# Optimization experiments

Hardware: AMD Instinct MI355X
Metric: run time of the kernel (lower is better)

Reference implementation:

```python
import jax, jax.numpy as jnp
import numpy as np

B, H, W, C = 16, 64, 64, 256
DIRECTIONS = [(0, -1), (1, -1), (1, 0), (1, 1), (0, 1), (-1, 1), (-1, 0), (-1, -1)]


def _shift(g, dx, dy):
    # zero-padded shift matching the torch _shift_grid semantics:
    # result[:, max(0,dy):H+min(0,dy), max(0,dx):W+min(0,dx)] = g[src slices]
    _, h, w, _ = g.shape
    padded = jnp.pad(g, ((0, 0), (max(0, dy), max(0, -dy)), (max(0, dx), max(0, -dx)), (0, 0)))
    return padded[:, max(0, -dy):max(0, -dy) + h, max(0, -dx):max(0, -dx) + w, :]


def setup_inputs() -> dict:
    key = jax.random.key(0)
    k1, k2, k3, k4 = jax.random.split(key, 4)
    grid_embedding = jax.random.normal(k1, (B, H, W, C), dtype=jnp.float32)
    Wd = jax.random.normal(k2, (8, C, C), dtype=jnp.float32) * 0.01  # per-direction weights
    Wc = jax.random.normal(k3, (C, 8 * C), dtype=jnp.float32) * 0.02  # Linear weight [out, in]
    bc = jax.random.normal(k4, (C,), dtype=jnp.float32) * 0.02
    return {"grid_embedding": grid_embedding, "Wd": Wd, "Wc": Wc, "bc": bc}


def reference(grid_embedding, Wd, Wc, bc):
    # stack the 8 zero-padded shifted copies: [8, B, H, W, C]
    shifted = jnp.stack([_shift(grid_embedding, dx, dy) for (dx, dy) in DIRECTIONS], axis=0)
    # per-direction channel matmul: [B, H, W, 8, C] (d-major over last two dims matches torch.cat order)
    proc = jnp.einsum('dbhwc,dce->bhwde', shifted, Wd)
    combined = proc.reshape(grid_embedding.shape[0], grid_embedding.shape[1], grid_embedding.shape[2], -1)
    # nn.Linear: y = x @ W.T + b
    return combined @ Wc.T + bc
```

## Files before the change

### kernel.cpp

```cpp
#include <hip/hip_runtime.h>


typedef unsigned short u16;
typedef unsigned int u32;
typedef __attribute__((ext_vector_type(8))) short bf16x8;
typedef __attribute__((ext_vector_type(4))) float f32x4;

#define GP_BYTES 35684352

__device__ __forceinline__ u16 f2bf(float f) {
  u32 u = __float_as_uint(f);
  u32 r = u + 0x7fffu + ((u >> 16) & 1u);
  return (u16)(r >> 16);
}
__device__ __forceinline__ u32 pack2(float a, float b) {
  return (u32)f2bf(a) | ((u32)f2bf(b) << 16);
}

__global__ __launch_bounds__(256) void pad_convert(const float* __restrict__ g,
                                                   u16* __restrict__ gp) {
  int id = blockIdx.x * 256 + threadIdx.x;
  if (id >= 2230272) return;
  int c8 = id & 31;
  int t = id >> 5;
  int xx = t % 66;
  int s = t / 66;
  int yy = s % 66;
  int b  = s / 66;
  u32 o0 = 0, o1 = 0, o2 = 0, o3 = 0;
  if (yy != 0 && yy != 65 && xx != 0 && xx != 65) {
    const float* src = g + ((((b << 6) + yy - 1) << 6) + xx - 1) * 256 + (c8 << 3);
    float4 fa = *(const float4*)src;
    float4 fb = *(const float4*)(src + 4);
    o0 = pack2(fa.x, fa.y);
    o1 = pack2(fa.z, fa.w);
    o2 = pack2(fb.x, fb.y);
    o3 = pack2(fb.z, fb.w);
  }
  uint4 v; v.x = o0; v.y = o1; v.z = o2; v.w = o3;
  *(uint4*)(gp + (size_t)id * 8) = v;
}

__global__ __launch_bounds__(256) void build_mt(const float* __restrict__ Wd,
                                                const float* __restrict__ Wc,
                                                u16* __restrict__ Bf) {
  __shared__ __align__(16) u16 As[128 * 32];
  __shared__ __align__(16) u16 Bs[128 * 32];
  const int bid = blockIdx.x;
  const int n0    = (bid & 1) << 7;
  const int mblk  = bid >> 1;
  const int d     = mblk >> 1;
  const int chalf = (mblk & 1) << 7;
  const int tid  = threadIdx.x;
  const int lane = tid & 63, wid = tid >> 6;
  const int wm = (wid >> 1) << 6, wn = (wid & 1) << 6;
  const int quad = lane >> 4, r16 = lane & 15;
  const int srow = tid >> 1, hh = tid & 1;
  const int swz  = (srow >> 1) & 3;
  const int ssl  = (quad ^ ((r16 >> 1) & 3)) << 3;
  f32x4 acc[4][4] = {};

  for (int e0 = 0; e0 < 256; e0 += 32) {
    __syncthreads();
    const float* pa = Wd + (size_t)(d * 256 + chalf + srow) * 256 + e0 + hh * 16;
    const float* pb = Wc + (size_t)(n0 + srow) * 2048 + d * 256 + e0 + hh * 16;
#pragma unroll
    for (int i = 0; i < 2; ++i) {
      float4 a0 = *(const float4*)(pa + i * 8);
      float4 a1 = *(const float4*)(pa + i * 8 + 4);
      float4 b0 = *(const float4*)(pb + i * 8);
      float4 b1 = *(const float4*)(pb + i * 8 + 4);
      uint4 va, vb;
      va.x = pack2(a0.x, a0.y); va.y = pack2(a0.z, a0.w);
      va.z = pack2(a1.x, a1.y); va.w = pack2(a1.z, a1.w);
      vb.x = pack2(b0.x, b0.y); vb.y = pack2(b0.z, b0.w);
      vb.z = pack2(b1.x, b1.y); vb.w = pack2(b1.z, b1.w);
      int slot = (2 * hh + i) ^ swz;
      *(uint4*)&As[srow * 32 + slot * 8] = va;
      *(uint4*)&Bs[srow * 32 + slot * 8] = vb;
    }
    __syncthreads();
    bf16x8 bfr[4];
#pragma unroll
    for (int nt = 0; nt < 4; ++nt)
      bfr[nt] = *(const bf16x8*)&Bs[(wn + nt * 16 + r16) * 32 + ssl];
#pragma unroll
    for (int mt = 0; mt < 4; ++mt) {
      bf16x8 af = *(const bf16x8*)&As[(wm + mt * 16 + r16) * 32 + ssl];
#pragma unroll
      for (int nt = 0; nt < 4; ++nt)
        acc[mt][nt] = __builtin_amdgcn_mfma_f32_16x16x32_bf16(af, bfr[nt], acc[mt][nt], 0, 0, 0);
    }
  }
#pragma unroll
  for (int mt = 0; mt < 4; ++mt) {
#pragma unroll
    for (int nt = 0; nt < 4; ++nt) {
      const int o = n0 + wn + nt * 16 + r16;
      f32x4 v = acc[mt][nt];
#pragma unroll
      for (int r = 0; r < 4; ++r) {
        const int c = chalf + wm + mt * 16 + quad * 4 + r;
        const int lane2 = (o & 15) + (((c >> 3) & 3) << 4);
        const size_t idx = ((size_t)((d * 8 + (c >> 5)) * 16 + (o >> 4)) * 512) + lane2 * 8 + (c & 7);
        Bf[idx] = f2bf(v[r]);
      }
    }
  }
}

__device__ __forceinline__ void async16(const u16* g, u16* l) {
  __builtin_amdgcn_global_load_lds((const __attribute__((address_space(1))) u32*)g,
                                   (__attribute__((address_space(3))) u32*)l, 16, 0, 0);
}

__global__ __launch_bounds__(512, 2) void conv_gemm(const u16* __restrict__ gp,
                                                    const u16* __restrict__ Bf,
                                                    const float* __restrict__ bc,
                                                    float* __restrict__ out) {
  __shared__ __align__(16) u16 slab[3][12800];
  const int bid = blockIdx.x;
  const int id2 = ((bid & 7) << 5) | (bid >> 3);
  const int b   = id2 >> 4;
  const int y0  = (id2 & 15) << 2;

  const int tid  = threadIdx.x;
  const int lane = tid & 63;
  const int wid  = tid >> 6;
  const int wm   = (wid >> 2) << 7;
  const int wn   = (wid & 3) << 6;
  const int quad = lane >> 4;
  const int r16  = lane & 15;

  const int i0 = tid, i1 = tid + 512, i2 = tid + 1024, i3 = 1536 + lane;
  const u16 *p0, *p1, *p2, *p3;
  {
    const size_t rowb = (size_t)(b * 66 + y0) * 66;
    int s, c;
    s = i0 >> 2; c = (i0 & 3) ^ ((s >> 1) & 3);
    p0 = gp + (rowb + (s / 66) * 66 + (s % 66)) * 256 + c * 8;
    s = i1 >> 2; c = (i1 & 3) ^ ((s >> 1) & 3);
    p1 = gp + (rowb + (s / 66) * 66 + (s % 66)) * 256 + c * 8;
    s = i2 >> 2; c = (i2 & 3) ^ ((s >> 1) & 3);
    p2 = gp + (rowb + (s / 66) * 66 + (s % 66)) * 256 + c * 8;
    s = i3 >> 2; c = (i3 & 3) ^ ((s >> 1) & 3);
    p3 = gp + (rowb + (s / 66) * 66 + (s % 66)) * 256 + c * 8;
  }
  const int l0 = i0 * 8, l1 = i1 * 8, l2 = i2 * 8, l3 = i3 * 8;

  const u16* baseBf = Bf + ((wn >> 4) << 9) + lane * 8;

  const int swm = (wm >> 6) * 66 + r16;
  const int q8  = quad << 3;

  constexpr int KLO[8] = {133, 132, 66,  0,  1,  2,  68, 134};
  constexpr int KHI[8] = {199, 198, 132, 66, 67, 68, 134, 200};
  constexpr int LBO[8] = {2 * 65536, 3 * 65536, 4 * 65536, 5 * 65536,
                          6 * 65536, 7 * 65536, 8192, 8192 + 65536};

  f32x4 acc[8][4] = {};
  bf16x8 Be[4], Bo[4];
  bf16x8 afl[4], afh[4];

  auto issueSlab = [&](u16* dst, int ch) {
    async16(p0 + ch, dst + l0);
    async16(p1 + ch, dst + l1);
    async16(p2 + ch, dst + l2);
    async16(p3 + ch, dst + l3);
  };
  auto loadB = [&](const u16* pB, int off, bf16x8* dst) {
#pragma unroll
    for (int nt = 0; nt < 4; ++nt) dst[nt] = *(const bf16x8*)(pB + off + nt * 512);
  };
  auto readAh = [&](const u16* bufR, int K, bf16x8* af) {
    const int s  = swm + K;
    const int sw = q8 ^ (((s >> 1) & 3) << 3);
    const u16* p = bufR + s * 32 + sw;
#pragma unroll
    for (int mt = 0; mt < 4; ++mt) af[mt] = *(const bf16x8*)(p + mt * 512);
  };
  auto mfma_half = [&](const bf16x8* af, const bf16x8* bb, int h) {
    __builtin_amdgcn_s_setprio(1);
#pragma unroll
    for (int mt = 0; mt < 4; ++mt)
#pragma unroll
      for (int nt = 0; nt < 4; ++nt)
        acc[h * 4 + mt][nt] =
            __builtin_amdgcn_mfma_f32_16x16x32_bf16(af[mt], bb[nt], acc[h * 4 + mt][nt], 0, 0, 0);
    __builtin_amdgcn_s_setprio(0);
  };

  auto stage_core = [&](const u16* bufR, const u16* pB, bool tailLoads) {
#pragma unroll
    for (int d = 0; d < 8; ++d) {
      bf16x8* bu = (d & 1) ? Bo : Be;
      readAh(bufR, KHI[d], afh);
      mfma_half(afl, bu, 0);
      if (d < 7) readAh(bufR, KLO[d + 1], afl);
      mfma_half(afh, bu, 1);
      if (d < 6 || tailLoads) loadB(pB, LBO[d], bu);
    }
  };

  issueSlab(slab[0], 0);
  loadB(baseBf, 0, Be);
  loadB(baseBf, 65536, Bo);
  issueSlab(slab[1], 32);
  asm volatile("s_waitcnt vmcnt(12)" ::: "memory");
  asm volatile("s_barrier" ::: "memory");
  readAh(slab[0], KLO[0], afl);

  const u16* pB = baseBf;
  u16* bR = slab[0]; u16* bN = slab[1]; u16* bT = slab[2];
#pragma unroll 1
  for (int cb = 0; cb < 6; ++cb) {
    stage_core(bR, pB, true);
    issueSlab(bT, (cb + 2) * 32);
    asm volatile("s_waitcnt vmcnt(12)" ::: "memory");
    asm volatile("s_barrier" ::: "memory");
    readAh(bN, KLO[0], afl);
    u16* t = bR; bR = bN; bN = bT; bT = t;
    pB += 8192;
  }
  stage_core(bR, pB, true);
  asm volatile("s_waitcnt vmcnt(8)" ::: "memory");
  asm volatile("s_barrier" ::: "memory");
  readAh(bN, KLO[0], afl);
  pB += 8192;
  stage_core(bN, pB, false);

  const int pbase = (b * 64 + y0) * 64;
#pragma unroll
  for (int nt = 0; nt < 4; ++nt) {
    const int o = wn + nt * 16 + r16;
    const float bias = bc[o];
#pragma unroll
    for (int mt = 0; mt < 8; ++mt) {
      const int pr = pbase + wm + mt * 16 + quad * 4;
      f32x4 v = acc[mt][nt];
#pragma unroll
      for (int r = 0; r < 4; ++r)
        out[(size_t)(pr + r) * 256 + o] = v[r] + bias;
    }
  }
}

extern "C" void kernel_launch(void* const* d_in, const int* in_sizes, int n_in,
                              void* d_out, int out_size, void* d_ws, size_t ws_size,
                              hipStream_t stream) {
  const float* g  = (const float*)d_in[0];
  const float* Wd = (const float*)d_in[1];
  const float* Wc = (const float*)d_in[2];
  const float* bc = (const float*)d_in[3];
  float* out = (float*)d_out;
  u16* gp = (u16*)d_ws;
  u16* Bf = (u16*)((char*)d_ws + GP_BYTES);

  pad_convert<<<8712, 256, 0, stream>>>(g, gp);
  build_mt<<<32, 256, 0, stream>>>(Wd, Wc, Bf);
  conv_gemm<<<256, 512, 0, stream>>>(gp, Bf, bc, out);
}
```

Baseline: 181.9 us.

## Fuse pad and bf16 conversion into conv GEMM slab loading

Removes the separate pad_convert kernel and the padded bf16 copy of the input. The GEMM kernel now reads fp32 activations directly, handles the zero-padding border with clamped addresses and masks, converts to bf16 in registers, and writes into a double-buffered LDS slab, with the loads spread across the MFMA subphases. This saves one kernel launch and the write and re-read of a large intermediate, at the cost of replacing the async global-to-LDS triple-buffer pipeline with register-staged double buffering and more VGPR pressure. It also vectorizes the bf16 stores in build_mt.

Result: slower. 282.5 us (+55.4%).

```diff
diff --git a/kernel.cpp b/kernel.cpp
--- a/kernel.cpp
+++ b/kernel.cpp
@@ -6,8 +6,6 @@
 typedef __attribute__((ext_vector_type(8))) short bf16x8;
 typedef __attribute__((ext_vector_type(4))) float f32x4;
 
-#define GP_BYTES 35684352
-
 __device__ __forceinline__ u16 f2bf(float f) {
   u32 u = __float_as_uint(f);
   u32 r = u + 0x7fffu + ((u >> 16) & 1u);
@@ -15,30 +13,6 @@
 }
 __device__ __forceinline__ u32 pack2(float a, float b) {
   return (u32)f2bf(a) | ((u32)f2bf(b) << 16);
-}
-
-__global__ __launch_bounds__(256) void pad_convert(const float* __restrict__ g,
-                                                   u16* __restrict__ gp) {
-  int id = blockIdx.x * 256 + threadIdx.x;
-  if (id >= 2230272) return;
-  int c8 = id & 31;
-  int t = id >> 5;
-  int xx = t % 66;
-  int s = t / 66;
-  int yy = s % 66;
-  int b  = s / 66;
-  u32 o0 = 0, o1 = 0, o2 = 0, o3 = 0;
-  if (yy != 0 && yy != 65 && xx != 0 && xx != 65) {
-    const float* src = g + ((((b << 6) + yy - 1) << 6) + xx - 1) * 256 + (c8 << 3);
-    float4 fa = *(const float4*)src;
-    float4 fb = *(const float4*)(src + 4);
-    o0 = pack2(fa.x, fa.y);
-    o1 = pack2(fa.z, fa.w);
-    o2 = pack2(fb.x, fb.y);
-    o3 = pack2(fb.z, fb.w);
-  }
-  uint4 v; v.x = o0; v.y = o1; v.z = o2; v.w = o3;
-  *(uint4*)(gp + (size_t)id * 8) = v;
 }
 
 __global__ __launch_bounds__(256) void build_mt(const float* __restrict__ Wd,
@@ -97,28 +71,22 @@
 #pragma unroll
     for (int nt = 0; nt < 4; ++nt) {
       const int o = n0 + wn + nt * 16 + r16;
+      const int c0 = chalf + wm + mt * 16 + quad * 4;
+      const int lane2 = (o & 15) + (((c0 >> 3) & 3) << 4);
+      const size_t idx0 = ((size_t)((d * 8 + (c0 >> 5)) * 16 + (o >> 4)) * 512) + lane2 * 8 + (c0 & 7);
       f32x4 v = acc[mt][nt];
-#pragma unroll
-      for (int r = 0; r < 4; ++r) {
-        const int c = chalf + wm + mt * 16 + quad * 4 + r;
-        const int lane2 = (o & 15) + (((c >> 3) & 3) << 4);
-        const size_t idx = ((size_t)((d * 8 + (c >> 5)) * 16 + (o >> 4)) * 512) + lane2 * 8 + (c & 7);
-        Bf[idx] = f2bf(v[r]);
-      }
-    }
-  }
-}
-
-__device__ __forceinline__ void async16(const u16* g, u16* l) {
-  __builtin_amdgcn_global_load_lds((const __attribute__((address_space(1))) u32*)g,
-                                   (__attribute__((address_space(3))) u32*)l, 16, 0, 0);
-}
-
-__global__ __launch_bounds__(512, 2) void conv_gemm(const u16* __restrict__ gp,
+      ushort4 w;
+      w.x = f2bf(v[0]); w.y = f2bf(v[1]); w.z = f2bf(v[2]); w.w = f2bf(v[3]);
+      *(ushort4*)&Bf[idx0] = w;
+    }
+  }
+}
+
+__global__ __launch_bounds__(512, 2) void conv_gemm(const float* __restrict__ g,
                                                     const u16* __restrict__ Bf,
                                                     const float* __restrict__ bc,
                                                     float* __restrict__ out) {
-  __shared__ __align__(16) u16 slab[3][12800];
+  __shared__ __align__(16) u16 slab[2][12672];
   const int bid = blockIdx.x;
   const int id2 = ((bid & 7) << 5) | (bid >> 3);
   const int b   = id2 >> 4;
@@ -132,21 +100,23 @@
   const int quad = lane >> 4;
   const int r16  = lane & 15;
 
-  const int i0 = tid, i1 = tid + 512, i2 = tid + 1024, i3 = 1536 + lane;
-  const u16 *p0, *p1, *p2, *p3;
-  {
-    const size_t rowb = (size_t)(b * 66 + y0) * 66;
-    int s, c;
-    s = i0 >> 2; c = (i0 & 3) ^ ((s >> 1) & 3);
-    p0 = gp + (rowb + (s / 66) * 66 + (s % 66)) * 256 + c * 8;
-    s = i1 >> 2; c = (i1 & 3) ^ ((s >> 1) & 3);
-    p1 = gp + (rowb + (s / 66) * 66 + (s % 66)) * 256 + c * 8;
-    s = i2 >> 2; c = (i2 & 3) ^ ((s >> 1) & 3);
-    p2 = gp + (rowb + (s / 66) * 66 + (s % 66)) * 256 + c * 8;
-    s = i3 >> 2; c = (i3 & 3) ^ ((s >> 1) & 3);
-    p3 = gp + (rowb + (s / 66) * 66 + (s % 66)) * 256 + c * 8;
-  }
-  const int l0 = i0 * 8, l1 = i1 * 8, l2 = i2 * 8, l3 = i3 * 8;
+  const bool has3 = (tid < 48);
+  int   ldso[4];
+  bool  bd[4];
+  const float* gsrc[4];
+#pragma unroll
+  for (int j = 0; j < 4; ++j) {
+    const int k = (j < 3) ? (tid + (j << 9)) : (1536 + tid);
+    const int s = k >> 2, slot = k & 3;
+    const int cs = slot ^ ((s >> 1) & 3);
+    const int sy = s / 66, sx = s % 66;
+    const int Y  = y0 + sy;
+    bd[j] = (sx == 0) | (sx == 65) | (Y == 0) | (Y == 65);
+    const int Yc = Y < 1 ? 1 : (Y > 64 ? 64 : Y);
+    const int xc = sx < 1 ? 1 : (sx > 64 ? 64 : sx);
+    gsrc[j] = g + ((size_t)(((b << 6) + Yc - 1) << 6) + (xc - 1)) * 256 + cs * 8;
+    ldso[j] = k * 8;
+  }
 
   const u16* baseBf = Bf + ((wn >> 4) << 9) + lane * 8;
 
@@ -162,11 +132,19 @@
   bf16x8 Be[4], Bo[4];
   bf16x8 afl[4], afh[4];
 
-  auto issueSlab = [&](u16* dst, int ch) {
-    async16(p0 + ch, dst + l0);
-    async16(p1 + ch, dst + l1);
-    async16(p2 + ch, dst + l2);
-    async16(p3 + ch, dst + l3);
+  auto loadChunk = [&](int j, int cho, float4& a, float4& c) {
+    a = make_float4(0.f, 0.f, 0.f, 0.f);
+    c = make_float4(0.f, 0.f, 0.f, 0.f);
+    if (!bd[j]) {
+      a = *(const float4*)(gsrc[j] + cho);
+      c = *(const float4*)(gsrc[j] + cho + 4);
+    }
+  };
+  auto writeChunk = [&](u16* bufW, int j, const float4& a, const float4& c) {
+    uint4 w;
+    w.x = pack2(a.x, a.y); w.y = pack2(a.z, a.w);
+    w.z = pack2(c.x, c.y); w.w = pack2(c.z, c.w);
+    *(uint4*)&bufW[ldso[j]] = w;
   };
   auto loadB = [&](const u16* pB, int off, bf16x8* dst) {
 #pragma unroll
@@ -189,45 +167,70 @@
             __builtin_amdgcn_mfma_f32_16x16x32_bf16(af[mt], bb[nt], acc[h * 4 + mt][nt], 0, 0, 0);
     __builtin_amdgcn_s_setprio(0);
   };
-
-  auto stage_core = [&](const u16* bufR, const u16* pB, bool tailLoads) {
-#pragma unroll
-    for (int d = 0; d < 8; ++d) {
-      bf16x8* bu = (d & 1) ? Bo : Be;
-      readAh(bufR, KHI[d], afh);
-      mfma_half(afl, bu, 0);
-      if (d < 7) readAh(bufR, KLO[d + 1], afl);
-      mfma_half(afh, bu, 1);
-      if (d < 6 || tailLoads) loadB(pB, LBO[d], bu);
-    }
-  };
-
-  issueSlab(slab[0], 0);
+  auto subphase = [&](const u16* bufR, const u16* pB, int d, bool nextAfl, bool doB) {
+    bf16x8* bu = (d & 1) ? Bo : Be;
+    readAh(bufR, KHI[d], afh);
+    mfma_half(afl, bu, 0);
+    if (nextAfl) readAh(bufR, KLO[d + 1], afl);
+    mfma_half(afh, bu, 1);
+    if (doB) loadB(pB, LBO[d], bu);
+  };
+
   loadB(baseBf, 0, Be);
   loadB(baseBf, 65536, Bo);
-  issueSlab(slab[1], 32);
-  asm volatile("s_waitcnt vmcnt(12)" ::: "memory");
+  {
+    float4 a0, c0, a1, c1, a2, c2, a3, c3;
+    loadChunk(0, 0, a0, c0);
+    loadChunk(1, 0, a1, c1);
+    loadChunk(2, 0, a2, c2);
+    if (has3) loadChunk(3, 0, a3, c3);
+    writeChunk(slab[0], 0, a0, c0);
+    writeChunk(slab[0], 1, a1, c1);
+    writeChunk(slab[0], 2, a2, c2);
+    if (has3) writeChunk(slab[0], 3, a3, c3);
+  }
+  asm volatile("s_waitcnt lgkmcnt(0)" ::: "memory");
   asm volatile("s_barrier" ::: "memory");
   readAh(slab[0], KLO[0], afl);
 
   const u16* pB = baseBf;
-  u16* bR = slab[0]; u16* bN = slab[1]; u16* bT = slab[2];
+  u16* bufR = slab[0];
+  u16* bufW = slab[1];
 #pragma unroll 1
-  for (int cb = 0; cb < 6; ++cb) {
-    stage_core(bR, pB, true);
-    issueSlab(bT, (cb + 2) * 32);
-    asm volatile("s_waitcnt vmcnt(12)" ::: "memory");
+  for (int cb = 0; cb < 7; ++cb) {
+    const int cho = (cb + 1) * 32;
+    float4 a0, c0, a1, c1;
+    loadChunk(0, cho, a0, c0);
+    loadChunk(1, cho, a1, c1);
+    subphase(bufR, pB, 0, true, true);
+    subphase(bufR, pB, 1, true, true);
+    subphase(bufR, pB, 2, true, true);
+    subphase(bufR, pB, 3, true, true);
+    writeChunk(bufW, 0, a0, c0);
+    writeChunk(bufW, 1, a1, c1);
+    float4 a2, c2, a3, c3;
+    loadChunk(2, cho, a2, c2);
+    if (has3) loadChunk(3, cho, a3, c3);
+    subphase(bufR, pB, 4, true, true);
+    subphase(bufR, pB, 5, true, true);
+    subphase(bufR, pB, 6, true, true);
+    subphase(bufR, pB, 7, false, true);
+    writeChunk(bufW, 2, a2, c2);
+    if (has3) writeChunk(bufW, 3, a3, c3);
+    asm volatile("s_waitcnt lgkmcnt(0)" ::: "memory");
     asm volatile("s_barrier" ::: "memory");
-    readAh(bN, KLO[0], afl);
-    u16* t = bR; bR = bN; bN = bT; bT = t;
+    readAh(bufW, KLO[0], afl);
+    u16* t = bufR; bufR = bufW; bufW = t;
     pB += 8192;
   }
-  stage_core(bR, pB, true);
-  asm volatile("s_waitcnt vmcnt(8)" ::: "memory");
-  asm volatile("s_barrier" ::: "memory");
-  readAh(bN, KLO[0], afl);
-  pB += 8192;
-  stage_core(bN, pB, false);
+  subphase(bufR, pB, 0, true, true);
+  subphase(bufR, pB, 1, true, true);
+  subphase(bufR, pB, 2, true, true);
+  subphase(bufR, pB, 3, true, true);
+  subphase(bufR, pB, 4, true, true);
+  subphase(bufR, pB, 5, true, true);
+  subphase(bufR, pB, 6, true, false);
+  subphase(bufR, pB, 7, false, false);
 
   const int pbase = (b * 64 + y0) * 64;
 #pragma unroll
@@ -253,10 +256,8 @@
   const float* Wc = (const float*)d_in[2];
   const float* bc = (const float*)d_in[3];
   float* out = (float*)d_out;
-  u16* gp = (u16*)d_ws;
-  u16* Bf = (u16*)((char*)d_ws + GP_BYTES);
-
-  pad_convert<<<8712, 256, 0, stream>>>(g, gp);
+  u16* Bf = (u16*)d_ws;
+
   build_mt<<<32, 256, 0, stream>>>(Wd, Wc, Bf);
-  conv_gemm<<<256, 512, 0, stream>>>(gp, Bf, bc, out);
-}
+  conv_gemm<<<256, 512, 0, stream>>>(g, Bf, bc, out);
+}
```
